# Performance work log

Measured on AMD Instinct MI355X. Metric: run time of the kernel, lower is better.

Reference implementation:

```python
import jax, jax.numpy as jnp
import numpy as np

SMALL = -1000.0


def setup_inputs() -> dict:
    key = jax.random.key(0)
    k1, k2, k3, k4 = jax.random.split(key, 4)
    B, T, L = 256, 1024, 64
    pred = jax.random.normal(k1, (B, T, L), dtype=jnp.float32)
    seq_len = jax.random.randint(k2, (B,), T // 2, T + 1)  # lengths in [T/2, T]
    ref = jax.random.randint(k3, (B, T), 0, L)
    # zero-pad tags beyond seq_len (required by the original end-tag indexing trick)
    ref = jnp.where(jnp.arange(T)[None, :] < seq_len[:, None], ref, 0)
    transitions = jax.random.normal(k4, (L + 2, L + 2), dtype=jnp.float32) * 0.1
    return {"pred": pred, "transitions": transitions, "ref": ref, "seq_len": seq_len}


def crf_neg_log_likelihood(pred, transitions, ref, seq_len):
    B, T, L = pred.shape
    dt = pred.dtype
    # --- build padded observations [B, T+2, L+2] ---
    obs_mid = jnp.concatenate([pred, jnp.full((B, T, 2), SMALL, dt)], axis=2)
    b_s = jnp.concatenate([jnp.full((L,), SMALL), jnp.array([0.0, SMALL])]).astype(dt)
    r_p = jnp.concatenate([jnp.zeros((L,)), jnp.array([SMALL, SMALL])]).astype(dt)
    obs = jnp.concatenate(
        [jnp.broadcast_to(b_s, (B, 1, L + 2)), obs_mid, jnp.broadcast_to(r_p, (B, 1, L + 2))],
        axis=1,
    )
    e_s = jnp.concatenate([jnp.full((L,), SMALL), jnp.array([0.0, 1000.0])]).astype(dt)
    obs = obs.at[jnp.arange(B), seq_len + 1].add(e_s)

    # --- forward algorithm: logsumexp recurrence over time ---
    def step(prev, ob):  # prev [B, L+2], ob [B, L+2]
        new = jax.nn.logsumexp(prev[:, :, None] + ob[:, None, :] + transitions[None], axis=1)
        return new, new

    prev0 = obs[:, 0]
    obs_t = jnp.swapaxes(obs[:, 1:], 0, 1)  # [T+1, B, L+2] time-major
    _, paths = jax.lax.scan(step, prev0, obs_t)  # paths [T+1, B, L+2]
    all_paths_scores = jax.nn.logsumexp(paths[seq_len, jnp.arange(B)], axis=1).sum()

    # --- gold path score ---
    mask = (jnp.arange(T)[None, :] < seq_len[:, None]).astype(dt)
    gold_emit = jnp.sum(jnp.take_along_axis(pred, ref[..., None], axis=2)[..., 0] * mask)
    padded = jnp.concatenate(
        [jnp.full((B, 1), L, ref.dtype), ref, jnp.zeros((B, 1), ref.dtype)], axis=1
    )  # [B, T+2]
    padded = padded.at[jnp.arange(B), seq_len + 1].add(L + 1)  # end tag id = L+1
    trans_sc = transitions[padded[:, :-1], padded[:, 1:]]  # [B, T+1]
    mask2 = (jnp.arange(T + 1)[None, :] < (seq_len + 1)[:, None]).astype(dt)
    gold = gold_emit + jnp.sum(trans_sc * mask2)
    return all_paths_scores - gold


def reference(pred, transitions, ref, seq_len):
    return crf_neg_log_likelihood(pred, transitions, ref, seq_len)
```

## Files before the change

kernel.cpp:

```cpp
#include <hip/hip_runtime.h>
#include <hip/hip_bf16.h>


#define RL_F(x, i) __uint_as_float(__builtin_amdgcn_readlane(__float_as_uint(x), (i)))
#define L2E 1.44269504088896340736f
#define LN2 0.69314718055994530942f

#define V_ALL(M) M(0) M(1) M(2) M(3) M(4) M(5) M(6) M(7) M(8) M(9) M(10) M(11) \
 M(12) M(13) M(14) M(15) M(16) M(17) M(18) M(19) M(20) M(21) M(22) M(23) M(24) \
 M(25) M(26) M(27) M(28) M(29) M(30) M(31) M(32) M(33) M(34) M(35) M(36) M(37) \
 M(38) M(39) M(40) M(41) M(42) M(43) M(44) M(45) M(46) M(47) M(48) M(49) M(50) \
 M(51) M(52) M(53) M(54) M(55) M(56) M(57) M(58) M(59) M(60) M(61) M(62) M(63)

#define DECLV(q) float V##q;
#define LOADF(q) V##q = __builtin_amdgcn_exp2f(tcol[(q) * 66] * L2E);
#define LOADB(q) V##q = __builtin_amdgcn_exp2f(trow[(q)] * L2E);
#define PINV(q)  asm volatile("" : "+v"(V##q));

#define FMA4(a,b,c,d) \
    s0 = fmaf(RL_F(x,a), V##a, s0); s1 = fmaf(RL_F(x,b), V##b, s1); \
    s2 = fmaf(RL_F(x,c), V##c, s2); s3 = fmaf(RL_F(x,d), V##d, s3);
#define FMA_ALL \
    FMA4(0,1,2,3)     FMA4(4,5,6,7)     FMA4(8,9,10,11)   FMA4(12,13,14,15) \
    FMA4(16,17,18,19) FMA4(20,21,22,23) FMA4(24,25,26,27) FMA4(28,29,30,31) \
    FMA4(32,33,34,35) FMA4(36,37,38,39) FMA4(40,41,42,43) FMA4(44,45,46,47) \
    FMA4(48,49,50,51) FMA4(52,53,54,55) FMA4(56,57,58,59) FMA4(60,61,62,63)

#define ROWF(i) pb[(((i) < 0) ? 0 : (((i) > 1023) ? 1023 : (i))) * 64]
#define EXPE(p) __builtin_amdgcn_exp2f((p) * L2E)

#define STEPN(E) { \
    float x = FWD ? a : a * (E); \
    float s0 = 0.f, s1 = 0.f, s2 = 0.f, s3 = 0.f; \
    FMA_ALL \
    float s = (s0 + s1) + (s2 + s3); \
    a = FWD ? s * (E) : s; }

#define RENORM { \
    unsigned abits = (unsigned)__builtin_amdgcn_readfirstlane((int)__float_as_uint(a)); \
    int k = (int)((abits >> 23) & 255u) - 127; \
    K += k; \
    a *= __uint_as_float((unsigned)(127 - k) << 23); }

template<bool FWD>
__device__ __forceinline__ void chain(const float* __restrict__ pred,
                                      const float* __restrict__ trans,
                                      int b, int lane, int sl, int h,
                                      float* __restrict__ wsV,
                                      int* __restrict__ wsK)
{
    const float* pb   = pred + (size_t)b * 65536 + lane;
    const float* tcol = trans + lane;
    const float* trow = trans + lane * 66;
    (void)tcol; (void)trow;

    V_ALL(DECLV)
    if (FWD) { V_ALL(LOADF) } else { V_ALL(LOADB) }
    V_ALL(PINV)

    float a;
    int   K = 0;
    if (FWD) a = __builtin_amdgcn_exp2f((pb[0] + trans[64 * 66 + lane]) * L2E);
    else     a = __builtin_amdgcn_exp2f(trow[65] * L2E);

    const int dir = FWD ? 1 : -1;
    int n = FWD ? h - 1 : sl - h;
    int r = FWD ? 1 : sl - 1;

    float E0 = EXPE(ROWF(r)), E1 = EXPE(ROWF(r + dir)),
          E2 = EXPE(ROWF(r + 2 * dir)), E3 = EXPE(ROWF(r + 3 * dir));
    while (n >= 4) {
        float F0 = ROWF(r + 4 * dir), F1 = ROWF(r + 5 * dir),
              F2 = ROWF(r + 6 * dir), F3 = ROWF(r + 7 * dir);
        STEPN(E0) STEPN(E1) STEPN(E2) STEPN(E3)
        RENORM
        E0 = EXPE(F0); E1 = EXPE(F1); E2 = EXPE(F2); E3 = EXPE(F3);
        r += 4 * dir; n -= 4;
    }
    if (n > 0) { STEPN(E0) --n; }
    if (n > 0) { STEPN(E1) --n; }
    if (n > 0) { STEPN(E2) }
    RENORM

    wsV[b * 64 + lane] = a;
    if (lane == 0) wsK[b] = K;
}

__global__ __launch_bounds__(64) __attribute__((amdgpu_waves_per_eu(1, 1)))
void chain_kernel(const float* __restrict__ pred,
                  const float* __restrict__ trans,
                  const int*   __restrict__ ref,
                  const int*   __restrict__ seqlen,
                  float* __restrict__ wsA, float* __restrict__ wsB,
                  int* __restrict__ wsKf, int* __restrict__ wsKb,
                  float* __restrict__ out)
{
    const int role = blockIdx.x >> 8;
    const int b    = blockIdx.x & 255;
    const int lane = threadIdx.x;
    const int sl   = seqlen[b];
    const int h    = (sl + 1) >> 1;

    if (role == 0) {
        chain<true>(pred, trans, b, lane, sl, h, wsA, wsKf);
    } else if (role == 1) {
        chain<false>(pred, trans, b, lane, sl, h, wsB, wsKb);
    } else {
        const int*   rb = ref  + b * 1024;
        const float* pg = pred + (size_t)b * 65536;
        float acc = 0.f;
        for (int t = lane; t <= sl; t += 64) {
            int from = (t == 0) ? 64 : rb[t - 1];
            int cur  = (t < sl) ? rb[t] : 65;
            acc += trans[from * 66 + cur];
            if (t < sl) acc += pg[t * 64 + cur];
        }
        #pragma unroll
        for (int off = 32; off; off >>= 1) acc += __shfl_xor(acc, off, 64);
        if (lane == 0) atomicAdd(out, -acc);
    }
}

__global__ __launch_bounds__(64) void combine_kernel(
    const float* __restrict__ wsA, const float* __restrict__ wsB,
    const int* __restrict__ wsKf, const int* __restrict__ wsKb,
    float* __restrict__ out)
{
    const int b = blockIdx.x, lane = threadIdx.x;
    float z = wsA[b * 64 + lane] * wsB[b * 64 + lane];
    #pragma unroll
    for (int off = 32; off; off >>= 1) z += __shfl_xor(z, off, 64);
    if (lane == 0) {
        float res = LN2 * (__builtin_amdgcn_logf(z) + (float)(wsKf[b] + wsKb[b]));
        atomicAdd(out, res);
    }
}

extern "C" void kernel_launch(void* const* d_in, const int* in_sizes, int n_in,
                              void* d_out, int out_size, void* d_ws, size_t ws_size,
                              hipStream_t stream) {
    const float* pred   = (const float*)d_in[0];
    const float* trans  = (const float*)d_in[1];
    const int*   ref    = (const int*)d_in[2];
    const int*   seqlen = (const int*)d_in[3];
    float* out = (float*)d_out;

    float* wsA  = (float*)d_ws;
    float* wsB  = wsA + 256 * 64;
    int*   wsKf = (int*)(wsB + 256 * 64);
    int*   wsKb = wsKf + 256;

    hipMemsetAsync(out, 0, sizeof(float), stream);
    chain_kernel<<<768, 64, 0, stream>>>(pred, trans, ref, seqlen,
                                         wsA, wsB, wsKf, wsKb, out);
    combine_kernel<<<256, 64, 0, stream>>>(wsA, wsB, wsKf, wsKb, out);
}
```

Measured before the change: 209.5 us.

## Use packed fp16 dot2 for CRF forward/backward matvec with per-step max renormalization

Replaces the 64 fp32 readlane+FMA per step with 32 packed-half readlanes and v_dot2 instructions, using transition weights exp-converted to fp16 pairs. To keep values in fp16 range, each step now renormalizes by the wave-wide max exponent computed via butterfly shuffles instead of renormalizing once every four steps from lane 0. This halves the serial readlane/FMA chain, but adds shuffle latency per step and reduces precision to fp16 inputs, which risks accuracy loss on the log-likelihood.

```diff
diff --git a/kernel.cpp b/kernel.cpp
--- a/kernel.cpp
+++ b/kernel.cpp
@@ -1,46 +1,64 @@
 #include <hip/hip_runtime.h>
 #include <hip/hip_bf16.h>
+#include <hip/hip_fp16.h>
 
 
-#define RL_F(x, i) __uint_as_float(__builtin_amdgcn_readlane(__float_as_uint(x), (i)))
+typedef _Float16 h2 __attribute__((ext_vector_type(2)));
+#define B2U(x) __builtin_bit_cast(unsigned, x)
+#define U2H(x) __builtin_bit_cast(h2, x)
 #define L2E 1.44269504088896340736f
 #define LN2 0.69314718055994530942f
+#define EXPE(p) __builtin_amdgcn_exp2f((p) * L2E)
 
-#define V_ALL(M) M(0) M(1) M(2) M(3) M(4) M(5) M(6) M(7) M(8) M(9) M(10) M(11) \
+#define W_ALL(M) M(0) M(1) M(2) M(3) M(4) M(5) M(6) M(7) M(8) M(9) M(10) M(11) \
  M(12) M(13) M(14) M(15) M(16) M(17) M(18) M(19) M(20) M(21) M(22) M(23) M(24) \
- M(25) M(26) M(27) M(28) M(29) M(30) M(31) M(32) M(33) M(34) M(35) M(36) M(37) \
- M(38) M(39) M(40) M(41) M(42) M(43) M(44) M(45) M(46) M(47) M(48) M(49) M(50) \
- M(51) M(52) M(53) M(54) M(55) M(56) M(57) M(58) M(59) M(60) M(61) M(62) M(63)
+ M(25) M(26) M(27) M(28) M(29) M(30) M(31)
 
-#define DECLV(q) float V##q;
-#define LOADF(q) V##q = __builtin_amdgcn_exp2f(tcol[(q) * 66] * L2E);
-#define LOADB(q) V##q = __builtin_amdgcn_exp2f(trow[(q)] * L2E);
-#define PINV(q)  asm volatile("" : "+v"(V##q));
+#define DECLW(q) unsigned W##q;
+#define LOADF(q) W##q = B2U(__builtin_amdgcn_cvt_pkrtz(EXPE(tcol[(2*(q))*66]), EXPE(tcol[(2*(q)+1)*66])));
+#define LOADB(q) W##q = B2U(__builtin_amdgcn_cvt_pkrtz(EXPE(trow[2*(q)]), EXPE(trow[2*(q)+1])));
+#define PINW(q)  asm volatile("" : "+v"(W##q));
 
-#define FMA4(a,b,c,d) \
-    s0 = fmaf(RL_F(x,a), V##a, s0); s1 = fmaf(RL_F(x,b), V##b, s1); \
-    s2 = fmaf(RL_F(x,c), V##c, s2); s3 = fmaf(RL_F(x,d), V##d, s3);
-#define FMA_ALL \
-    FMA4(0,1,2,3)     FMA4(4,5,6,7)     FMA4(8,9,10,11)   FMA4(12,13,14,15) \
-    FMA4(16,17,18,19) FMA4(20,21,22,23) FMA4(24,25,26,27) FMA4(28,29,30,31) \
-    FMA4(32,33,34,35) FMA4(36,37,38,39) FMA4(40,41,42,43) FMA4(44,45,46,47) \
-    FMA4(48,49,50,51) FMA4(52,53,54,55) FMA4(56,57,58,59) FMA4(60,61,62,63)
+#define RLD(q) int u##q = __builtin_amdgcn_readlane((int)P, 2*(q));
+#define RL_ALL W_ALL(RLD)
+
+#if __has_builtin(__builtin_amdgcn_fdot2)
+#define DOTQ(q, acc) acc = __builtin_amdgcn_fdot2(U2H((unsigned)u##q), U2H(W##q), acc, false);
+#else
+#define DOTQ(q, acc) { h2 _u = U2H((unsigned)u##q), _w = U2H(W##q); \
+    acc = fmaf((float)_u[0], (float)_w[0], fmaf((float)_u[1], (float)_w[1], acc)); }
+#endif
+#define DOT_ALL \
+    DOTQ(0,s0)  DOTQ(1,s1)  DOTQ(2,s2)  DOTQ(3,s3)  DOTQ(4,s0)  DOTQ(5,s1) \
+    DOTQ(6,s2)  DOTQ(7,s3)  DOTQ(8,s0)  DOTQ(9,s1)  DOTQ(10,s2) DOTQ(11,s3) \
+    DOTQ(12,s0) DOTQ(13,s1) DOTQ(14,s2) DOTQ(15,s3) DOTQ(16,s0) DOTQ(17,s1) \
+    DOTQ(18,s2) DOTQ(19,s3) DOTQ(20,s0) DOTQ(21,s1) DOTQ(22,s2) DOTQ(23,s3) \
+    DOTQ(24,s0) DOTQ(25,s1) DOTQ(26,s2) DOTQ(27,s3) DOTQ(28,s0) DOTQ(29,s1) \
+    DOTQ(30,s2) DOTQ(31,s3)
+
+#define BMAX(m) \
+    m = fmaxf(m, __shfl_xor(m, 1, 64));  m = fmaxf(m, __shfl_xor(m, 2, 64)); \
+    m = fmaxf(m, __shfl_xor(m, 4, 64));  m = fmaxf(m, __shfl_xor(m, 8, 64)); \
+    m = fmaxf(m, __shfl_xor(m, 16, 64)); m = fmaxf(m, __shfl_xor(m, 32, 64));
+
+#define EXPO_OF(m) ((int)(((unsigned)__builtin_amdgcn_readfirstlane((int)__float_as_uint(m)) >> 23) & 255u) - 127)
 
 #define ROWF(i) pb[(((i) < 0) ? 0 : (((i) > 1023) ? 1023 : (i))) * 64]
-#define EXPE(p) __builtin_amdgcn_exp2f((p) * L2E)
 
-#define STEPN(E) { \
-    float x = FWD ? a : a * (E); \
+#define STEPX(E) { \
+    float sc = __uint_as_float((unsigned)(127 - k) << 23); \
+    K += k; \
+    float x = FWD ? a * sc : (a * sc) * (E); \
+    float xo = __shfl_xor(x, 1, 64); \
+    unsigned P = B2U(__builtin_amdgcn_cvt_pkrtz(x, xo)); \
+    RL_ALL \
     float s0 = 0.f, s1 = 0.f, s2 = 0.f, s3 = 0.f; \
-    FMA_ALL \
+    DOT_ALL \
+    float m = x; \
+    BMAX(m) \
+    k = EXPO_OF(m); \
     float s = (s0 + s1) + (s2 + s3); \
     a = FWD ? s * (E) : s; }
-
-#define RENORM { \
-    unsigned abits = (unsigned)__builtin_amdgcn_readfirstlane((int)__float_as_uint(a)); \
-    int k = (int)((abits >> 23) & 255u) - 127; \
-    K += k; \
-    a *= __uint_as_float((unsigned)(127 - k) << 23); }
 
 template<bool FWD>
 __device__ __forceinline__ void chain(const float* __restrict__ pred,
@@ -54,14 +72,18 @@
     const float* trow = trans + lane * 66;
     (void)tcol; (void)trow;
 
-    V_ALL(DECLV)
-    if (FWD) { V_ALL(LOADF) } else { V_ALL(LOADB) }
-    V_ALL(PINV)
+    W_ALL(DECLW)
+    if (FWD) { W_ALL(LOADF) } else { W_ALL(LOADB) }
+    W_ALL(PINW)
 
     float a;
     int   K = 0;
     if (FWD) a = __builtin_amdgcn_exp2f((pb[0] + trans[64 * 66 + lane]) * L2E);
     else     a = __builtin_amdgcn_exp2f(trow[65] * L2E);
+
+    float m0 = a;
+    BMAX(m0)
+    int k = EXPO_OF(m0);
 
     const int dir = FWD ? 1 : -1;
     int n = FWD ? h - 1 : sl - h;
@@ -72,15 +94,13 @@
     while (n >= 4) {
         float F0 = ROWF(r + 4 * dir), F1 = ROWF(r + 5 * dir),
               F2 = ROWF(r + 6 * dir), F3 = ROWF(r + 7 * dir);
-        STEPN(E0) STEPN(E1) STEPN(E2) STEPN(E3)
-        RENORM
+        STEPX(E0) STEPX(E1) STEPX(E2) STEPX(E3)
         E0 = EXPE(F0); E1 = EXPE(F1); E2 = EXPE(F2); E3 = EXPE(F3);
         r += 4 * dir; n -= 4;
     }
-    if (n > 0) { STEPN(E0) --n; }
-    if (n > 0) { STEPN(E1) --n; }
-    if (n > 0) { STEPN(E2) }
-    RENORM
+    if (n > 0) { STEPX(E0) --n; }
+    if (n > 0) { STEPX(E1) --n; }
+    if (n > 0) { STEPX(E2) }
 
     wsV[b * 64 + lane] = a;
     if (lane == 0) wsK[b] = K;
```

Measured after the change: 257.2 us. +22.8%, slower.
